# Performance work log

Measured on AMD Instinct MI355X. Metric: run time of the kernel, lower is better.

The kernel has to match this reference:

```python
import jax, jax.numpy as jnp
import numpy as np

T = 4096          # prefill tokens (single sequence)
HK = 16           # key heads
HV = 32           # value heads
DK = 128          # key head dim
DV = 128          # value head dim
K = 4             # causal conv kernel width
QKV = 2 * HK * DK + HV * DV  # 8192


def setup_inputs() -> dict:
    key = jax.random.key(0)
    k1, k2, k3, k4, k5, k6 = jax.random.split(key, 6)
    return {
        "mixed_qkv": jax.random.normal(k1, (T, QKV), dtype=jnp.float32),
        "a": jax.random.normal(k2, (T, HV), dtype=jnp.float32),
        "b": jax.random.normal(k3, (T, HV), dtype=jnp.float32),
        "conv_w": jax.random.normal(k4, (QKV, K), dtype=jnp.float32) * 0.2,
        "dt_bias": jax.random.normal(k5, (HV,), dtype=jnp.float32),
        "alog": jax.random.normal(k6, (HV,), dtype=jnp.float32),
    }


def _l2norm(x, eps=1e-6):
    return x * jax.lax.rsqrt(jnp.sum(x * x, axis=-1, keepdims=True) + eps)


def _forward(mixed_qkv, a, b, conv_w, dt_bias, alog):
    # --- causal depthwise conv1d (zero initial conv state) + SiLU ---
    xp = jnp.pad(mixed_qkv, ((K - 1, 0), (0, 0)))  # [T+K-1, QKV]
    y = sum(conv_w[None, :, j] * xp[j:j + T] for j in range(K))  # [T, QKV]
    x = jax.nn.silu(y)

    # --- split q/k/v ---
    q, k_, v = jnp.split(x, [HK * DK, 2 * HK * DK], axis=-1)
    q = q.reshape(T, HK, DK)
    k_ = k_.reshape(T, HK, DK)
    v = v.reshape(T, HV, DV)

    # use_qk_l2norm_in_kernel=True: L2-norm q,k; scale q by dk^-0.5
    q = _l2norm(q) * (DK ** -0.5)
    k_ = _l2norm(k_)

    # GQA: repeat key-head q/k to value-head count
    grp = HV // HK
    q = jnp.repeat(q, grp, axis=1)   # [T, HV, DK]
    k_ = jnp.repeat(k_, grp, axis=1)  # [T, HV, DK]

    # --- fused_gdn_gating ---
    g = -jnp.exp(alog)[None, :] * jax.nn.softplus(a + dt_bias[None, :])  # [T, HV]
    beta = jax.nn.sigmoid(b)                                             # [T, HV]

    # --- gated delta-rule recurrence (equiv. to chunk_gated_delta_rule) ---
    S0 = jnp.zeros((HV, DK, DV), dtype=mixed_qkv.dtype)

    def step(S, inp):
        qt, kt, vt, gt, bt = inp
        S = S * jnp.exp(gt)[:, None, None]                 # gated decay
        pred = jnp.einsum('hk,hkv->hv', kt, S)             # k^T S
        delta = (vt - pred) * bt[:, None]                  # beta-scaled error
        S = S + jnp.einsum('hk,hv->hkv', kt, delta)        # delta update
        o = jnp.einsum('hk,hkv->hv', qt, S)                # query readout
        return S, o

    _, out = jax.lax.scan(step, S0, (q, k_, v, g, beta))
    return out  # [T, HV, DV]


def reference(mixed_qkv, a, b, conv_w, dt_bias, alog):
    return _forward(mixed_qkv, a, b, conv_w, dt_bias, alog)
```

## Files before the change

kernel.cpp:

```cpp
#include <hip/hip_runtime.h>

#define T_LEN 4096
#define HKn   16
#define HVn   32
#define DKn   128
#define DVn   128
#define QKVn  8192
#define NCH   64
#define CS    64

typedef __attribute__((ext_vector_type(8))) short short8;
typedef __attribute__((ext_vector_type(4))) float f32x4;

#define OFF_QSH  ((size_t)0)
#define OFF_QSL  ((size_t)16777216)
#define OFF_KSH  ((size_t)33554432)
#define OFF_KSL  ((size_t)50331648)
#define OFF_KTH  ((size_t)67108864)
#define OFF_KTL  ((size_t)83886080)
#define OFF_VA   ((size_t)100663296)
#define OFF_GBL  ((size_t)167772160)
#define OFF_G    ((size_t)168820736)
#define OFF_WH   ((size_t)169345024)
#define OFF_WL   ((size_t)202899456)
#define OFF_MH   ((size_t)236453888)
#define OFF_ML   ((size_t)253231104)

template <int CTRL>
__device__ __forceinline__ float dpp_add(float x) {
    int v = __builtin_amdgcn_update_dpp(0, __float_as_int(x), CTRL, 0xF, 0xF, true);
    return x + __int_as_float(v);
}
__device__ __forceinline__ float reduce32g(float x) {
    x = dpp_add<0x128>(x); x = dpp_add<0x124>(x);
    x = dpp_add<0x122>(x); x = dpp_add<0x121>(x);
    int v = __builtin_amdgcn_ds_swizzle(__float_as_int(x), 0x401F);
    return x + __int_as_float(v);
}
__device__ __forceinline__ unsigned short bf16rne(float f) {
    unsigned x = __float_as_uint(f);
    return (unsigned short)((x + 0x7FFFu + ((x >> 16) & 1u)) >> 16);
}
__device__ __forceinline__ float bf16tof(unsigned short h) {
    return __uint_as_float(((unsigned)h) << 16);
}
__device__ __forceinline__ void bsplit(float f, unsigned short& h, unsigned short& l) {
    h = bf16rne(f);
    l = bf16rne(f - bf16tof(h));
}
__device__ __forceinline__ f32x4 MF(short8 a, short8 b, f32x4 c) {
    return __builtin_amdgcn_mfma_f32_16x16x32_bf16(a, b, c, 0, 0, 0);
}
#define SB0() __builtin_amdgcn_sched_barrier(0)

__global__ __launch_bounds__(256) void k_gate(
    const float* __restrict__ a, const float* __restrict__ b,
    const float* __restrict__ dt_bias, const float* __restrict__ alog,
    float2* __restrict__ gbl)
{
    const int i = blockIdx.x * 256 + threadIdx.x;
    if (i < T_LEN * HVn) {
        const int h = i >> 12, t = i & (T_LEN - 1);
        const float av = a[(size_t)t * HVn + h];
        const float bv = b[(size_t)t * HVn + h];
        const float xv = av + dt_bias[h];
        const float sp = fmaxf(xv, 0.f) + log1pf(expf(-fabsf(xv)));
        const float g  = -expf(alog[h]) * sp;
        const float beta = 1.f / (1.f + expf(-bv));
        gbl[(size_t)h * T_LEN + t] = make_float2(beta, g);
    }
}

__global__ __launch_bounds__(128) void k_conv(
    const float* __restrict__ x, const float* __restrict__ w,
    const float* __restrict__ bgate,
    unsigned short* __restrict__ qsh, unsigned short* __restrict__ qsl,
    unsigned short* __restrict__ ksh, unsigned short* __restrict__ ksl,
    float* __restrict__ va2)
{
    const int t = blockIdx.x, seg = blockIdx.y, d = threadIdx.x;
    const int c = seg * 128 + d;
    const float4 w4 = ((const float4*)w)[c];
    float acc;
    if (t >= 3) {
        const float* xc = x + (size_t)(t - 3) * QKVn + c;
        acc = fmaf(w4.x, xc[0], fmaf(w4.y, xc[(size_t)QKVn],
              fmaf(w4.z, xc[(size_t)2 * QKVn], w4.w * xc[(size_t)3 * QKVn])));
    } else {
        float a0 = (t - 3 >= 0) ? x[(size_t)(t - 3) * QKVn + c] : 0.f;
        float a1 = (t - 2 >= 0) ? x[(size_t)(t - 2) * QKVn + c] : 0.f;
        float a2 = (t - 1 >= 0) ? x[(size_t)(t - 1) * QKVn + c] : 0.f;
        float a3 = x[(size_t)t * QKVn + c];
        acc = fmaf(w4.x, a0, fmaf(w4.y, a1, fmaf(w4.z, a2, w4.w * a3)));
    }
    const float y = acc / (1.f + expf(-acc));

    if (seg < 32) {
        float ss = reduce32g(y * y);
        __shared__ float part[4];
        if ((threadIdx.x & 31) == 0) part[threadIdx.x >> 5] = ss;
        __syncthreads();
        const float total = part[0] + part[1] + part[2] + part[3];
        const float r = rsqrtf(total + 1e-6f);
        float o = y * r;
        unsigned short hh, ll;
        if (seg < 16) {
            o *= 0.08838834764831845f;
            bsplit(o, hh, ll);
            const size_t idx = ((size_t)seg * T_LEN + t) * DKn + d;
            qsh[idx] = hh; qsl[idx] = ll;
        } else {
            bsplit(o, hh, ll);
            const size_t idx = ((size_t)(seg - 16) * T_LEN + t) * DKn + d;
            ksh[idx] = hh; ksl[idx] = ll;
        }
    } else {
        const int h = seg - 32;
        const float bv = bgate[(size_t)t * HVn + h];
        const float beta = 1.f / (1.f + expf(-bv));
        va2[((size_t)h * T_LEN + t) * DVn + d] = y * beta;
    }
}

__global__ __launch_bounds__(256) void k_tr(
    const unsigned short* __restrict__ ksh, const unsigned short* __restrict__ ksl,
    unsigned short* __restrict__ kth, unsigned short* __restrict__ ktl)
{
    __shared__ unsigned pk[64][65];
    const int b = blockIdx.x;
    const int kh = b >> 7, tt = (b >> 1) & 63, hh = b & 1;
    const int t0 = tt * 64, d0 = hh * 64;
    const int tid = threadIdx.x;
    #pragma unroll
    for (int e = 0; e < 16; ++e) {
        const int lin = e * 256 + tid;
        const int tl = lin >> 6, dl = lin & 63;
        const size_t o = ((size_t)kh * T_LEN + t0 + tl) * DKn + d0 + dl;
        pk[tl][dl] = ((unsigned)ksh[o] << 16) | (unsigned)ksl[o];
    }
    __syncthreads();
    #pragma unroll
    for (int e = 0; e < 16; ++e) {
        const int lin = e * 256 + tid;
        const int dl = lin >> 6, tl = lin & 63;
        const unsigned v = pk[tl][dl];
        const size_t o = ((size_t)kh * DKn + d0 + dl) * T_LEN + t0 + tl;
        kth[o] = (unsigned short)(v >> 16);
        ktl[o] = (unsigned short)(v & 0xFFFF);
    }
}

__global__ __launch_bounds__(256) void k_p1(
    const float2* __restrict__ gbl,
    const unsigned short* __restrict__ qsh, const unsigned short* __restrict__ qsl,
    const unsigned short* __restrict__ ksh, const unsigned short* __restrict__ ksl,
    float* __restrict__ va2, float* __restrict__ Gbuf,
    unsigned short* __restrict__ Wh, unsigned short* __restrict__ Wl,
    unsigned short* __restrict__ Mh, unsigned short* __restrict__ Ml)
{
    __shared__ float sA[64][68];
    __shared__ float sG[64];
    __shared__ float sB[64];
    const int blk = blockIdx.x;
    const int h = blk >> 6, ch = blk & 63;
    const int kh = h >> 1, t0 = ch * 64;
    const int tid = threadIdx.x, lane = tid & 63, wid = tid >> 6;
    const int l15 = lane & 15, lg = lane >> 4;

    if (tid < 64) {
        float2 g2 = gbl[(size_t)h * T_LEN + t0 + tid];
        sB[tid] = g2.x;
        float G = g2.y;
        #pragma unroll
        for (int s = 1; s < 64; s <<= 1) {
            float y = __int_as_float(__builtin_amdgcn_ds_bpermute((tid - s) << 2, __float_as_int(G)));
            G += (tid >= s) ? y : 0.f;
        }
        sG[tid] = G;
        Gbuf[(size_t)h * T_LEN + t0 + tid] = G;
    }
    __syncthreads();

    const char TIa[10] = {0,1,1,2,2,2,3,3,3,3};
    const char TJa[10] = {0,0,1,0,1,2,0,1,2,3};
    const size_t kbase = ((size_t)kh * T_LEN + t0) * DKn;
    for (int idx = wid; idx < 10; idx += 4) {
        const int mi = TIa[idx], nj = TJa[idx];
        f32x4 aKK = {0.f,0.f,0.f,0.f}, aQK = {0.f,0.f,0.f,0.f};
        #pragma unroll
        for (int kk = 0; kk < 4; ++kk) {
            const size_t offA = kbase + (size_t)(16*mi + l15) * DKn + 32*kk + 8*lg;
            const size_t offB = kbase + (size_t)(16*nj + l15) * DKn + 32*kk + 8*lg;
            short8 kAh = *(const short8*)(ksh + offA);
            short8 kAl = *(const short8*)(ksl + offA);
            short8 kBh = *(const short8*)(ksh + offB);
            short8 kBl = *(const short8*)(ksl + offB);
            short8 qAh = *(const short8*)(qsh + offA);
            short8 qAl = *(const short8*)(qsl + offA);
            aKK = MF(kAh,kBh,aKK); aKK = MF(kAh,kBl,aKK); aKK = MF(kAl,kBh,aKK);
            aQK = MF(qAh,kBh,aQK); aQK = MF(qAh,kBl,aQK); aQK = MF(qAl,kBh,aQK);
        }
        #pragma unroll
        for (int r = 0; r < 4; ++r) {
            const int i = 16*mi + 4*lg + r;
            const int j = 16*nj + l15;
            const float e = __expf(fminf(sG[i] - sG[j], 0.f));
            sA[i][j] = (j < i) ? sB[i] * e * aKK[r] : 0.f;
            const float mv = (j <= i) ? e * aQK[r] : 0.f;
            unsigned short mh, ml; bsplit(mv, mh, ml);
            const size_t moff = (((size_t)h * NCH + ch) * CS + i) * CS + j;
            Mh[moff] = mh; Ml[moff] = ml;
        }
    }
    __syncthreads();

    const int c = tid;
    float X[64];
    if (c < 128) {
        #pragma unroll
        for (int i = 0; i < 64; ++i)
            X[i] = va2[((size_t)h * T_LEN + t0 + i) * DVn + c];
    } else {
        const int dk = c - 128;
        #pragma unroll
        for (int i = 0; i < 64; ++i) {
            const size_t o = ((size_t)kh * T_LEN + t0 + i) * DKn + dk;
            const float kf = bf16tof(ksh[o]) + bf16tof(ksl[o]);
            X[i] = sB[i] * __expf(sG[i]) * kf;
        }
    }
    #pragma unroll
    for (int i = 1; i < 64; ++i) {
        float acc = X[i];
        const int nq = (i + 3) >> 2;
        #pragma unroll
        for (int q = 0; q < nq; ++q) {
            const f32x4 aa = *(const f32x4*)&sA[i][4*q];
            acc = fmaf(-aa[0], X[4*q+0], acc);
            acc = fmaf(-aa[1], X[4*q+1], acc);
            acc = fmaf(-aa[2], X[4*q+2], acc);
            acc = fmaf(-aa[3], X[4*q+3], acc);
        }
        X[i] = acc;
    }
    if (c < 128) {
        #pragma unroll
        for (int i = 0; i < 64; ++i)
            va2[((size_t)h * T_LEN + t0 + i) * DVn + c] = X[i];
    } else {
        const int dk = c - 128;
        #pragma unroll
        for (int i = 0; i < 64; ++i) {
            unsigned short wh, wl; bsplit(-X[i], wh, wl);
            const size_t o = (((size_t)h * NCH + ch) * CS + i) * DKn + dk;
            Wh[o] = wh; Wl[o] = wl;
        }
    }
}

struct ChBuf {
    short8 qh[4], ql[4];
    short8 wh[4], wl[4];
    short8 mh[2], ml[2];
    short8 th[2][2], tl[2][2];
    float  u[4];
    float  gv;
};

__device__ __forceinline__ void issue_ch(ChBuf& B, int ch,
    const unsigned short* __restrict__ qsh, const unsigned short* __restrict__ qsl,
    const unsigned short* __restrict__ kth, const unsigned short* __restrict__ ktl,
    const unsigned short* __restrict__ Wh, const unsigned short* __restrict__ Wl,
    const unsigned short* __restrict__ Mh, const unsigned short* __restrict__ Ml,
    const float* __restrict__ va2, const float* __restrict__ Gbuf,
    int h, int kh, int n0, int wid, int l15, int lg, int tid)
{
    const int t0 = ch * CS;
    const size_t qbase = ((size_t)kh * T_LEN + t0 + 16*wid + l15) * DKn;
    #pragma unroll
    for (int kk = 0; kk < 4; ++kk) {
        B.qh[kk] = *(const short8*)(qsh + qbase + 32*kk + 8*lg);
        B.ql[kk] = *(const short8*)(qsl + qbase + 32*kk + 8*lg);
    }
    const size_t wbase = (((size_t)h * NCH + ch) * CS + 16*wid + l15) * DKn;
    #pragma unroll
    for (int kk = 0; kk < 4; ++kk) {
        B.wh[kk] = *(const short8*)(Wh + wbase + 32*kk + 8*lg);
        B.wl[kk] = *(const short8*)(Wl + wbase + 32*kk + 8*lg);
    }
    const size_t mbase = (((size_t)h * NCH + ch) * CS + 16*wid + l15) * CS;
    #pragma unroll
    for (int k2 = 0; k2 < 2; ++k2) {
        B.mh[k2] = *(const short8*)(Mh + mbase + 32*k2 + 8*lg);
        B.ml[k2] = *(const short8*)(Ml + mbase + 32*k2 + 8*lg);
    }
    #pragma unroll
    for (int m2 = 0; m2 < 2; ++m2) {
        const size_t kb2 = ((size_t)kh * DKn + 16*(wid + 4*m2) + l15) * T_LEN + t0;
        #pragma unroll
        for (int k2 = 0; k2 < 2; ++k2) {
            B.th[m2][k2] = *(const short8*)(kth + kb2 + 32*k2 + 8*lg);
            B.tl[m2][k2] = *(const short8*)(ktl + kb2 + 32*k2 + 8*lg);
        }
    }
    #pragma unroll
    for (int r = 0; r < 4; ++r)
        B.u[r] = va2[((size_t)h * T_LEN + t0 + 16*wid + 4*lg + r) * DVn + n0 + l15];
    B.gv = Gbuf[(size_t)h * T_LEN + t0 + (tid & 63)];
}

__device__ __forceinline__ void compute_ch(const ChBuf& B, int ch,
    float (*sS)[17], unsigned (*sDL)[17], unsigned (*sDS)[17],
    float* sG, float* sE, float* __restrict__ out,
    int h, int n0, int wid, int l15, int lg, int tid)
{
    const int t0 = ch * CS;
    if (tid < 64) sG[tid] = B.gv;
    __syncthreads();
    if (tid < 64) sE[tid] = __expf(sG[63] - sG[tid]);

    short8 Sh[4], Sl[4];
    #pragma unroll
    for (int kk = 0; kk < 4; ++kk) {
        #pragma unroll
        for (int j = 0; j < 8; ++j) {
            const float sv = sS[32*kk + 8*lg + j][l15];
            unsigned short hh, ll; bsplit(sv, hh, ll);
            Sh[kk][j] = (short)hh; Sl[kk][j] = (short)ll;
        }
    }
    f32x4 dl;
    #pragma unroll
    for (int r = 0; r < 4; ++r) dl[r] = B.u[r];
    #pragma unroll
    for (int kk = 0; kk < 4; ++kk) {
        dl = MF(B.wh[kk], Sh[kk], dl); dl = MF(B.wh[kk], Sl[kk], dl); dl = MF(B.wl[kk], Sh[kk], dl);
    }
    __syncthreads();

    #pragma unroll
    for (int r = 0; r < 4; ++r) {
        const int cc = 16*wid + 4*lg + r;
        unsigned short hh, ll;
        bsplit(dl[r], hh, ll);
        sDL[cc][l15] = ((unsigned)hh << 16) | ll;
        const float fs = dl[r] * sE[cc];
        bsplit(fs, hh, ll);
        sDS[cc][l15] = ((unsigned)hh << 16) | ll;
    }
    __syncthreads();

    f32x4 aq = {0.f,0.f,0.f,0.f}, am = {0.f,0.f,0.f,0.f};
    #pragma unroll
    for (int kk = 0; kk < 4; ++kk) {
        aq = MF(B.qh[kk], Sh[kk], aq); aq = MF(B.qh[kk], Sl[kk], aq); aq = MF(B.ql[kk], Sh[kk], aq);
    }
    #pragma unroll
    for (int k2 = 0; k2 < 2; ++k2) {
        short8 bh, bl;
        #pragma unroll
        for (int j = 0; j < 8; ++j) {
            const unsigned pk = sDL[32*k2 + 8*lg + j][l15];
            bh[j] = (short)(pk >> 16); bl[j] = (short)(pk & 0xFFFF);
        }
        am = MF(B.mh[k2], bh, am); am = MF(B.mh[k2], bl, am); am = MF(B.ml[k2], bh, am);
    }
    #pragma unroll
    for (int r = 0; r < 4; ++r) {
        const int cc = 16*wid + 4*lg + r;
        const float sc = __expf(sG[cc]);
        out[((size_t)(t0 + cc) * HVn + h) * DVn + n0 + l15] = fmaf(sc, aq[r], am[r]);
    }

    short8 bh2[2], bl2[2];
    #pragma unroll
    for (int k2 = 0; k2 < 2; ++k2) {
        #pragma unroll
        for (int j = 0; j < 8; ++j) {
            const unsigned pk = sDS[32*k2 + 8*lg + j][l15];
            bh2[k2][j] = (short)(pk >> 16); bl2[k2][j] = (short)(pk & 0xFFFF);
        }
    }
    const float lam = __expf(sG[63]);
    #pragma unroll
    for (int m2 = 0; m2 < 2; ++m2) {
        f32x4 t4 = {0.f,0.f,0.f,0.f};
        #pragma unroll
        for (int k2 = 0; k2 < 2; ++k2) {
            t4 = MF(B.th[m2][k2], bh2[k2], t4); t4 = MF(B.th[m2][k2], bl2[k2], t4); t4 = MF(B.tl[m2][k2], bh2[k2], t4);
        }
        #pragma unroll
        for (int r = 0; r < 4; ++r) {
            const int dk = 16*(wid + 4*m2) + 4*lg + r;
            sS[dk][l15] = fmaf(lam, sS[dk][l15], t4[r]);
        }
    }
    __syncthreads();
}

__global__ __launch_bounds__(256, 1) void k_p2(
    const unsigned short* __restrict__ qsh, const unsigned short* __restrict__ qsl,
    const unsigned short* __restrict__ kth, const unsigned short* __restrict__ ktl,
    const unsigned short* __restrict__ Wh, const unsigned short* __restrict__ Wl,
    const unsigned short* __restrict__ Mh, const unsigned short* __restrict__ Ml,
    const float* __restrict__ va2, const float* __restrict__ Gbuf,
    float* __restrict__ out)
{
    __shared__ float sS[128][17];
    __shared__ unsigned sDL[64][17];
    __shared__ unsigned sDS[64][17];
    __shared__ float sG[64];
    __shared__ float sE[64];

    const int p = blockIdx.x;
    const int slot = p >> 3;
    const int h  = (p & 7) * 4 + (slot & 3);
    const int nb = slot >> 2;
    const int kh = h >> 1, n0 = nb * 16;
    const int tid = threadIdx.x, lane = tid & 63, wid = tid >> 6;
    const int l15 = lane & 15, lg = lane >> 4;

    for (int z = tid; z < 128 * 17; z += 256) ((float*)sS)[z] = 0.f;
    __syncthreads();

    ChBuf bufA, bufB;
    issue_ch(bufA, 0, qsh, qsl, kth, ktl, Wh, Wl, Mh, Ml, va2, Gbuf,
             h, kh, n0, wid, l15, lg, tid);

    #pragma unroll 1
    for (int ch2 = 0; ch2 < NCH / 2; ++ch2) {
        const int ch = 2 * ch2;
        SB0();
        issue_ch(bufB, ch + 1, qsh, qsl, kth, ktl, Wh, Wl, Mh, Ml, va2, Gbuf,
                 h, kh, n0, wid, l15, lg, tid);
        SB0();
        compute_ch(bufA, ch, sS, sDL, sDS, sG, sE, out, h, n0, wid, l15, lg, tid);
        SB0();
        if (ch + 2 < NCH)
            issue_ch(bufA, ch + 2, qsh, qsl, kth, ktl, Wh, Wl, Mh, Ml, va2, Gbuf,
                     h, kh, n0, wid, l15, lg, tid);
        SB0();
        compute_ch(bufB, ch + 1, sS, sDL, sDS, sG, sE, out, h, n0, wid, l15, lg, tid);
    }
}

extern "C" void kernel_launch(void* const* d_in, const int* in_sizes, int n_in,
                              void* d_out, int out_size, void* d_ws, size_t ws_size,
                              hipStream_t stream) {
    const float* mixed_qkv = (const float*)d_in[0];
    const float* a         = (const float*)d_in[1];
    const float* b         = (const float*)d_in[2];
    const float* conv_w    = (const float*)d_in[3];
    const float* dt_bias   = (const float*)d_in[4];
    const float* alog      = (const float*)d_in[5];
    float* out = (float*)d_out;
    char* ws = (char*)d_ws;

    unsigned short* qsh = (unsigned short*)(ws + OFF_QSH);
    unsigned short* qsl = (unsigned short*)(ws + OFF_QSL);
    unsigned short* ksh = (unsigned short*)(ws + OFF_KSH);
    unsigned short* ksl = (unsigned short*)(ws + OFF_KSL);
    unsigned short* kth = (unsigned short*)(ws + OFF_KTH);
    unsigned short* ktl = (unsigned short*)(ws + OFF_KTL);
    float*  va2 = (float*)(ws + OFF_VA);
    float2* gbl = (float2*)(ws + OFF_GBL);
    float*  Gbf = (float*)(ws + OFF_G);
    unsigned short* Wh = (unsigned short*)(ws + OFF_WH);
    unsigned short* Wl = (unsigned short*)(ws + OFF_WL);
    unsigned short* Mh = (unsigned short*)(ws + OFF_MH);
    unsigned short* Ml = (unsigned short*)(ws + OFF_ML);

    k_gate<<<(T_LEN * HVn + 255) / 256, 256, 0, stream>>>(a, b, dt_bias, alog, gbl);

    dim3 cgrid(T_LEN, 64);
    k_conv<<<cgrid, 128, 0, stream>>>(mixed_qkv, conv_w, b, qsh, qsl, ksh, ksl, va2);

    k_tr<<<2048, 256, 0, stream>>>(ksh, ksl, kth, ktl);

    k_p1<<<HVn * NCH, 256, 0, stream>>>(gbl, qsh, qsl, ksh, ksl, va2, Gbf, Wh, Wl, Mh, Ml);

    k_p2<<<HVn * 8, 256, 0, stream>>>(qsh, qsl, kth, ktl, Wh, Wl, Mh, Ml, va2, Gbf, out);
}
```

Before: 555.3 us.

## Keep chunk state in registers and cut barriers in recurrence kernel

The per-chunk recurrence kernel now keeps the fp32 state slice in accumulator registers and its bf16 hi/lo split operands in registers. Shared memory only exchanges packed hi/lo words, using transposed layouts that allow 128-bit vector reads and writes plus perm-based unpacking. Gate values are loaded per lane directly from global memory instead of staged through shared memory. This cuts the number of barriers per chunk from four to two and removes scalar LDS gathers and repeated bf16 splits. In exchange it raises register pressure and relies on the new LDS layouts being free of bank conflicts.

```diff
diff --git a/kernel.cpp b/kernel.cpp
--- a/kernel.cpp
+++ b/kernel.cpp
@@ -11,6 +11,7 @@
 
 typedef __attribute__((ext_vector_type(8))) short short8;
 typedef __attribute__((ext_vector_type(4))) float f32x4;
+typedef __attribute__((ext_vector_type(4))) unsigned u32x4;
 
 #define OFF_QSH  ((size_t)0)
 #define OFF_QSL  ((size_t)16777216)
@@ -48,8 +49,24 @@
     h = bf16rne(f);
     l = bf16rne(f - bf16tof(h));
 }
+__device__ __forceinline__ unsigned packsplit(float f) {
+    unsigned short h, l; bsplit(f, h, l);
+    return ((unsigned)h << 16) | (unsigned)l;
+}
 __device__ __forceinline__ f32x4 MF(short8 a, short8 b, f32x4 c) {
     return __builtin_amdgcn_mfma_f32_16x16x32_bf16(a, b, c, 0, 0, 0);
+}
+__device__ __forceinline__ void unpack8(u32x4 x0, u32x4 x1, short8& hi, short8& lo) {
+    union { u32x4 u; short8 s; } H, L;
+    H.u[0] = __builtin_amdgcn_perm(x0.y, x0.x, 0x07060302u);
+    L.u[0] = __builtin_amdgcn_perm(x0.y, x0.x, 0x05040100u);
+    H.u[1] = __builtin_amdgcn_perm(x0.w, x0.z, 0x07060302u);
+    L.u[1] = __builtin_amdgcn_perm(x0.w, x0.z, 0x05040100u);
+    H.u[2] = __builtin_amdgcn_perm(x1.y, x1.x, 0x07060302u);
+    L.u[2] = __builtin_amdgcn_perm(x1.y, x1.x, 0x05040100u);
+    H.u[3] = __builtin_amdgcn_perm(x1.w, x1.z, 0x07060302u);
+    L.u[3] = __builtin_amdgcn_perm(x1.w, x1.z, 0x05040100u);
+    hi = H.s; lo = L.s;
 }
 #define SB0() __builtin_amdgcn_sched_barrier(0)
 
@@ -264,7 +281,8 @@
     short8 mh[2], ml[2];
     short8 th[2][2], tl[2][2];
     float  u[4];
-    float  gv;
+    float4 g4;
+    float  g63;
 };
 
 __device__ __forceinline__ void issue_ch(ChBuf& B, int ch,
@@ -273,7 +291,7 @@
     const unsigned short* __restrict__ Wh, const unsigned short* __restrict__ Wl,
     const unsigned short* __restrict__ Mh, const unsigned short* __restrict__ Ml,
     const float* __restrict__ va2, const float* __restrict__ Gbuf,
-    int h, int kh, int n0, int wid, int l15, int lg, int tid)
+    int h, int kh, int n0, int wid, int l15, int lg)
 {
     const int t0 = ch * CS;
     const size_t qbase = ((size_t)kh * T_LEN + t0 + 16*wid + l15) * DKn;
@@ -306,96 +324,90 @@
     #pragma unroll
     for (int r = 0; r < 4; ++r)
         B.u[r] = va2[((size_t)h * T_LEN + t0 + 16*wid + 4*lg + r) * DVn + n0 + l15];
-    B.gv = Gbuf[(size_t)h * T_LEN + t0 + (tid & 63)];
+    const float* gp = Gbuf + (size_t)h * T_LEN + t0;
+    B.g4  = *(const float4*)(gp + 16*wid + 4*lg);
+    B.g63 = gp[63];
 }
 
 __device__ __forceinline__ void compute_ch(const ChBuf& B, int ch,
-    float (*sS)[17], unsigned (*sDL)[17], unsigned (*sDS)[17],
-    float* sG, float* sE, float* __restrict__ out,
-    int h, int n0, int wid, int l15, int lg, int tid)
+    unsigned (*sSp)[132], unsigned (*sDLp)[68], unsigned (*sDSp)[68],
+    short8* Sbh, short8* Sbl, f32x4* Sc,
+    float* __restrict__ out,
+    int h, int n0, int wid, int l15, int lg)
 {
     const int t0 = ch * CS;
-    if (tid < 64) sG[tid] = B.gv;
+    const float g63 = B.g63;
+    const float gr[4] = {B.g4.x, B.g4.y, B.g4.z, B.g4.w};
+
+    f32x4 dl;
+    #pragma unroll
+    for (int r = 0; r < 4; ++r) dl[r] = B.u[r];
+    #pragma unroll
+    for (int kk = 0; kk < 4; ++kk) {
+        dl = MF(B.wh[kk], Sbh[kk], dl); dl = MF(B.wh[kk], Sbl[kk], dl); dl = MF(B.wl[kk], Sbh[kk], dl);
+    }
+
+    const int cc0 = 16*wid + 4*lg;
+    u32x4 pdl, pds;
+    #pragma unroll
+    for (int r = 0; r < 4; ++r) {
+        pdl[r] = packsplit(dl[r]);
+        pds[r] = packsplit(dl[r] * __expf(g63 - gr[r]));
+    }
+    *(u32x4*)&sDLp[l15][cc0] = pdl;
+    *(u32x4*)&sDSp[l15][cc0] = pds;
     __syncthreads();
-    if (tid < 64) sE[tid] = __expf(sG[63] - sG[tid]);
-
-    short8 Sh[4], Sl[4];
+
+    short8 dlh[2], dll[2], dsh[2], dsl[2];
+    #pragma unroll
+    for (int k2 = 0; k2 < 2; ++k2) {
+        u32x4 x0 = *(const u32x4*)&sDLp[l15][32*k2 + 8*lg];
+        u32x4 x1 = *(const u32x4*)&sDLp[l15][32*k2 + 8*lg + 4];
+        unpack8(x0, x1, dlh[k2], dll[k2]);
+        u32x4 y0 = *(const u32x4*)&sDSp[l15][32*k2 + 8*lg];
+        u32x4 y1 = *(const u32x4*)&sDSp[l15][32*k2 + 8*lg + 4];
+        unpack8(y0, y1, dsh[k2], dsl[k2]);
+    }
+
+    f32x4 aq = {0.f,0.f,0.f,0.f}, am = {0.f,0.f,0.f,0.f};
     #pragma unroll
     for (int kk = 0; kk < 4; ++kk) {
-        #pragma unroll
-        for (int j = 0; j < 8; ++j) {
-            const float sv = sS[32*kk + 8*lg + j][l15];
-            unsigned short hh, ll; bsplit(sv, hh, ll);
-            Sh[kk][j] = (short)hh; Sl[kk][j] = (short)ll;
-        }
-    }
-    f32x4 dl;
-    #pragma unroll
-    for (int r = 0; r < 4; ++r) dl[r] = B.u[r];
-    #pragma unroll
-    for (int kk = 0; kk < 4; ++kk) {
-        dl = MF(B.wh[kk], Sh[kk], dl); dl = MF(B.wh[kk], Sl[kk], dl); dl = MF(B.wl[kk], Sh[kk], dl);
-    }
-    __syncthreads();
-
+        aq = MF(B.qh[kk], Sbh[kk], aq); aq = MF(B.qh[kk], Sbl[kk], aq); aq = MF(B.ql[kk], Sbh[kk], aq);
+    }
+    #pragma unroll
+    for (int k2 = 0; k2 < 2; ++k2) {
+        am = MF(B.mh[k2], dlh[k2], am); am = MF(B.mh[k2], dll[k2], am); am = MF(B.ml[k2], dlh[k2], am);
+    }
     #pragma unroll
     for (int r = 0; r < 4; ++r) {
-        const int cc = 16*wid + 4*lg + r;
-        unsigned short hh, ll;
-        bsplit(dl[r], hh, ll);
-        sDL[cc][l15] = ((unsigned)hh << 16) | ll;
-        const float fs = dl[r] * sE[cc];
-        bsplit(fs, hh, ll);
-        sDS[cc][l15] = ((unsigned)hh << 16) | ll;
-    }
-    __syncthreads();
-
-    f32x4 aq = {0.f,0.f,0.f,0.f}, am = {0.f,0.f,0.f,0.f};
-    #pragma unroll
-    for (int kk = 0; kk < 4; ++kk) {
-        aq = MF(B.qh[kk], Sh[kk], aq); aq = MF(B.qh[kk], Sl[kk], aq); aq = MF(B.ql[kk], Sh[kk], aq);
-    }
-    #pragma unroll
-    for (int k2 = 0; k2 < 2; ++k2) {
-        short8 bh, bl;
-        #pragma unroll
-        for (int j = 0; j < 8; ++j) {
-            const unsigned pk = sDL[32*k2 + 8*lg + j][l15];
-            bh[j] = (short)(pk >> 16); bl[j] = (short)(pk & 0xFFFF);
-        }
-        am = MF(B.mh[k2], bh, am); am = MF(B.mh[k2], bl, am); am = MF(B.ml[k2], bh, am);
-    }
-    #pragma unroll
-    for (int r = 0; r < 4; ++r) {
-        const int cc = 16*wid + 4*lg + r;
-        const float sc = __expf(sG[cc]);
-        out[((size_t)(t0 + cc) * HVn + h) * DVn + n0 + l15] = fmaf(sc, aq[r], am[r]);
-    }
-
-    short8 bh2[2], bl2[2];
-    #pragma unroll
-    for (int k2 = 0; k2 < 2; ++k2) {
-        #pragma unroll
-        for (int j = 0; j < 8; ++j) {
-            const unsigned pk = sDS[32*k2 + 8*lg + j][l15];
-            bh2[k2][j] = (short)(pk >> 16); bl2[k2][j] = (short)(pk & 0xFFFF);
-        }
-    }
-    const float lam = __expf(sG[63]);
+        const int cc = cc0 + r;
+        out[((size_t)(t0 + cc) * HVn + h) * DVn + n0 + l15] = fmaf(__expf(gr[r]), aq[r], am[r]);
+    }
+
+    const float lam = __expf(g63);
     #pragma unroll
     for (int m2 = 0; m2 < 2; ++m2) {
         f32x4 t4 = {0.f,0.f,0.f,0.f};
         #pragma unroll
         for (int k2 = 0; k2 < 2; ++k2) {
-            t4 = MF(B.th[m2][k2], bh2[k2], t4); t4 = MF(B.th[m2][k2], bl2[k2], t4); t4 = MF(B.tl[m2][k2], bh2[k2], t4);
-        }
+            t4 = MF(B.th[m2][k2], dsh[k2], t4); t4 = MF(B.th[m2][k2], dsl[k2], t4); t4 = MF(B.tl[m2][k2], dsh[k2], t4);
+        }
+        u32x4 ps;
         #pragma unroll
         for (int r = 0; r < 4; ++r) {
-            const int dk = 16*(wid + 4*m2) + 4*lg + r;
-            sS[dk][l15] = fmaf(lam, sS[dk][l15], t4[r]);
-        }
+            Sc[m2][r] = fmaf(lam, Sc[m2][r], t4[r]);
+            ps[r] = packsplit(Sc[m2][r]);
+        }
+        *(u32x4*)&sSp[l15][16*wid + 64*m2 + 4*lg] = ps;
     }
     __syncthreads();
+
+    #pragma unroll
+    for (int kk = 0; kk < 4; ++kk) {
+        u32x4 z0 = *(const u32x4*)&sSp[l15][32*kk + 8*lg];
+        u32x4 z1 = *(const u32x4*)&sSp[l15][32*kk + 8*lg + 4];
+        unpack8(z0, z1, Sbh[kk], Sbl[kk]);
+    }
 }
 
 __global__ __launch_bounds__(256, 1) void k_p2(
@@ -406,11 +418,9 @@
     const float* __restrict__ va2, const float* __restrict__ Gbuf,
     float* __restrict__ out)
 {
-    __shared__ float sS[128][17];
-    __shared__ unsigned sDL[64][17];
-    __shared__ unsigned sDS[64][17];
-    __shared__ float sG[64];
-    __shared__ float sE[64];
+    __shared__ unsigned sSp[16][132];
+    __shared__ unsigned sDLp[16][68];
+    __shared__ unsigned sDSp[16][68];
 
     const int p = blockIdx.x;
     const int slot = p >> 3;
@@ -420,27 +430,32 @@
     const int tid = threadIdx.x, lane = tid & 63, wid = tid >> 6;
     const int l15 = lane & 15, lg = lane >> 4;
 
-    for (int z = tid; z < 128 * 17; z += 256) ((float*)sS)[z] = 0.f;
-    __syncthreads();
+    short8 Sbh[4], Sbl[4];
+    f32x4 Sc[2];
+    const short8 z8 = {0,0,0,0,0,0,0,0};
+    #pragma unroll
+    for (int kk = 0; kk < 4; ++kk) { Sbh[kk] = z8; Sbl[kk] = z8; }
+    Sc[0] = (f32x4){0.f,0.f,0.f,0.f};
+    Sc[1] = (f32x4){0.f,0.f,0.f,0.f};
 
     ChBuf bufA, bufB;
     issue_ch(bufA, 0, qsh, qsl, kth, ktl, Wh, Wl, Mh, Ml, va2, Gbuf,
-             h, kh, n0, wid, l15, lg, tid);
+             h, kh, n0, wid, l15, lg);
 
     #pragma unroll 1
     for (int ch2 = 0; ch2 < NCH / 2; ++ch2) {
         const int ch = 2 * ch2;
         SB0();
         issue_ch(bufB, ch + 1, qsh, qsl, kth, ktl, Wh, Wl, Mh, Ml, va2, Gbuf,
-                 h, kh, n0, wid, l15, lg, tid);
+                 h, kh, n0, wid, l15, lg);
         SB0();
-        compute_ch(bufA, ch, sS, sDL, sDS, sG, sE, out, h, n0, wid, l15, lg, tid);
+        compute_ch(bufA, ch, sSp, sDLp, sDSp, Sbh, Sbl, Sc, out, h, n0, wid, l15, lg);
         SB0();
         if (ch + 2 < NCH)
             issue_ch(bufA, ch + 2, qsh, qsl, kth, ktl, Wh, Wl, Mh, Ml, va2, Gbuf,
-                     h, kh, n0, wid, l15, lg, tid);
+                     h, kh, n0, wid, l15, lg);
         SB0();
-        compute_ch(bufB, ch + 1, sS, sDL, sDS, sG, sE, out, h, n0, wid, l15, lg, tid);
+        compute_ch(bufB, ch + 1, sSp, sDLp, sDSp, Sbh, Sbl, Sc, out, h, n0, wid, l15, lg);
     }
 }
 
```

Measured after the change: 531.0 us. -4.4%, faster.
